# Optimization experiments

Measured on AMD Instinct MI355X. Metric: run time of the kernel, lower is better.

Reference implementation:

```python
import jax, jax.numpy as jnp
import numpy as np

N = 4096
C = 64
B = 4
DIST_THRESHOLD = 0.5
ALPHA = 0.01
NEG_INF = -1e15


def setup_inputs() -> dict:
    key = jax.random.key(0)
    k1, k2, k3, k4, k5 = jax.random.split(key, 5)
    x = jax.random.normal(k1, (B, N, C), dtype=jnp.float32)
    dist_mat = jax.random.uniform(k2, (N, N), dtype=jnp.float32)
    proj_w = jax.random.normal(k3, (N, C, C), dtype=jnp.float32) / np.sqrt(C)
    proj_b = jax.random.normal(k4, (N, C), dtype=jnp.float32) * 0.01
    a_w = jax.random.normal(k5, (N, 2 * C), dtype=jnp.float32) / np.sqrt(2 * C)
    return {"x": x, "dist_mat": dist_mat, "proj_w": proj_w, "proj_b": proj_b, "a_w": a_w}


def reference(x, dist_mat, proj_w, proj_b, a_w):
    # Adjacency: (0 < dist < threshold), diagonal forced to 1.
    adj = (dist_mat > 0) & (dist_mat < DIST_THRESHOLD)
    adj = adj | jnp.eye(N, dtype=bool)

    # Per-node projection (GraphDense): h[b,n,:] = x[b,n,:] @ proj_w[n] + proj_b[n]
    h = jnp.einsum('bnc,nco->bno', x, proj_w) + proj_b  # [B, N, C]

    # Attention score: a[j] . concat(h_i, h_j) without materializing [B,N,N,2C].
    a_src, a_dst = a_w[:, :C], a_w[:, C:]               # each [N, C]
    s = jnp.einsum('bic,jc->bij', h, a_src) + jnp.einsum('bjc,jc->bj', h, a_dst)[:, None, :]
    s = jnp.where(s >= 0, s, ALPHA * s)                 # LeakyReLU
    s = jnp.where(adj[None, :, :], s, NEG_INF)          # mask non-edges
    att = jax.nn.softmax(s, axis=-1)                    # [B, N, N]

    # Weighted aggregation over neighbors.
    y = jnp.einsum('bij,bjc->bic', att, h)              # [B, N, C]
    return y
```

## Files before the change

### kernel.cpp

```cpp
#include <hip/hip_runtime.h>

#define N 4096
#define C 64
#define B 4
#define SHIFT 12.0f

typedef __attribute__((ext_vector_type(8))) short short8;
typedef __attribute__((ext_vector_type(4))) short s16x4;
typedef __attribute__((ext_vector_type(4))) float f32x4;
typedef unsigned long long u64;

#define MFMA16(a, b, c) __builtin_amdgcn_mfma_f32_16x16x32_bf16(a, b, c, 0, 0, 0)

__device__ __forceinline__ short f2bf(float f) {
    unsigned u = __builtin_bit_cast(unsigned, f);
    u += 0x7fffu + ((u >> 16) & 1u);
    return (short)(u >> 16);
}

__global__ __launch_bounds__(256) void mask_kernel(const float* __restrict__ dist,
                                                   u64* __restrict__ msk) {
    const int wave = threadIdx.x >> 6, lane = threadIdx.x & 63;
    const int i = blockIdx.x * 4 + wave;
    const float* row = dist + (size_t)i * N;
#pragma unroll 8
    for (int jb = 0; jb < N / 64; jb++) {
        float d = row[jb * 64 + lane];
        u64 m = __ballot(d > 0.f && d < 0.5f);
        int dj = i - jb * 64;
        if (dj >= 0 && dj < 64) m |= (1ull << dj);
        if (lane == 0) msk[(size_t)i * (N / 64) + jb] = m;
    }
}

__global__ __launch_bounds__(256) void proj_kernel(
    const float* __restrict__ x,
    const float* __restrict__ proj_w,
    const float* __restrict__ proj_b,
    const float* __restrict__ a_w,
    short* __restrict__ h_bf,
    short* __restrict__ a_srcb,
    float* __restrict__ e2)
{
    __shared__ float lds_x[4][B][C];

    const int tid = threadIdx.x;
    const int wave = tid >> 6;
    const int lane = tid & 63;
    const int g = lane >> 4;
    const int o4 = lane & 15;
    const int n = blockIdx.x * 4 + wave;
    const float* Wn = proj_w + (size_t)n * C * C;

#pragma unroll
    for (int b = 0; b < B; b++)
        lds_x[wave][b][lane] = x[((size_t)b * N + n) * C + lane];

    float4 wbuf[16];
#pragma unroll
    for (int p = 0; p < 16; p++)
        wbuf[p] = *(const float4*)(Wn + (p * 4 + g) * C + o4 * 4);

    float acc[B][4];
#pragma unroll
    for (int b = 0; b < B; b++)
#pragma unroll
        for (int r = 0; r < 4; r++) acc[b][r] = 0.f;

#pragma unroll
    for (int p = 0; p < 16; p++) {
        float xs[B];
#pragma unroll
        for (int b = 0; b < B; b++) xs[b] = lds_x[wave][b][p * 4 + g];
#pragma unroll
        for (int b = 0; b < B; b++) {
            acc[b][0] = fmaf(xs[b], wbuf[p].x, acc[b][0]);
            acc[b][1] = fmaf(xs[b], wbuf[p].y, acc[b][1]);
            acc[b][2] = fmaf(xs[b], wbuf[p].z, acc[b][2]);
            acc[b][3] = fmaf(xs[b], wbuf[p].w, acc[b][3]);
        }
    }

#pragma unroll
    for (int b = 0; b < B; b++)
#pragma unroll
        for (int r = 0; r < 4; r++) {
            acc[b][r] += __shfl_xor(acc[b][r], 16, 64);
            acc[b][r] += __shfl_xor(acc[b][r], 32, 64);
        }

    float4 pb4 = *(const float4*)(proj_b + (size_t)n * C + o4 * 4);
#pragma unroll
    for (int b = 0; b < B; b++) {
        acc[b][0] += pb4.x; acc[b][1] += pb4.y;
        acc[b][2] += pb4.z; acc[b][3] += pb4.w;
    }

    float hg[4];
#pragma unroll
    for (int r = 0; r < 4; r++) {
        float v01 = (g & 1) ? acc[1][r] : acc[0][r];
        float v23 = (g & 1) ? acc[3][r] : acc[2][r];
        hg[r] = (g & 2) ? v23 : v01;
    }

    {
        s16x4 hv;
#pragma unroll
        for (int r = 0; r < 4; r++) hv[r] = f2bf(hg[r]);
        *(s16x4*)&h_bf[((size_t)g * N + n) * C + o4 * 4] = hv;
    }

    if (g == 0) {
        float4 as4 = *(const float4*)(a_w + (size_t)n * 2 * C + o4 * 4);
        s16x4 av;
        av[0] = f2bf(as4.x); av[1] = f2bf(as4.y);
        av[2] = f2bf(as4.z); av[3] = f2bf(as4.w);
        *(s16x4*)&a_srcb[(size_t)n * C + o4 * 4] = av;
    }

    {
        float4 ad4 = *(const float4*)(a_w + (size_t)n * 2 * C + C + o4 * 4);
        float s = hg[0] * ad4.x + hg[1] * ad4.y + hg[2] * ad4.z + hg[3] * ad4.w;
        s += __shfl_xor(s, 1, 64);
        s += __shfl_xor(s, 2, 64);
        s += __shfl_xor(s, 4, 64);
        s += __shfl_xor(s, 8, 64);
        if (o4 == 0) e2[g * N + n] = s - SHIFT;
    }
}

__global__ __launch_bounds__(256) void transpose_kernel(const short* __restrict__ h_bf,
                                                        short* __restrict__ hT_bf) {
    __shared__ short tile[64][72];
    const int t = threadIdx.x;
    const int b = blockIdx.y;
    const int n0 = blockIdx.x * 64;
    {
        int r = t >> 2, cs = (t & 3) * 16;
        const short* src = h_bf + ((size_t)b * N + n0 + r) * C + cs;
#pragma unroll
        for (int q = 0; q < 4; q++)
            *(s16x4*)&tile[r][cs + q * 4] = *(const s16x4*)(src + q * 4);
    }
    __syncthreads();
    {
        int c = t >> 2, ns = (t & 3) * 16;
        short v[16];
#pragma unroll
        for (int k = 0; k < 16; k++) v[k] = tile[ns + k][c];
        short* dst = hT_bf + (size_t)b * C * N + (size_t)c * N + n0 + ns;
        *(short8*)dst = *(short8*)&v[0];
        *(short8*)(dst + 8) = *(short8*)&v[8];
    }
}

__global__ __launch_bounds__(256) void attn_kernel(
    const u64* __restrict__ msk,
    const short* __restrict__ h_bf,
    const short* __restrict__ hT_bf,
    const short* __restrict__ a_srcb,
    const float* __restrict__ e2,
    float* __restrict__ part_y,
    float* __restrict__ part_l,
    int JS, int S, int mode)
{
    __shared__ short lds_a[2][64][72];

    const int tid = threadIdx.x;
    const int wave = tid >> 6;
    const int lane = tid & 63;
    const int cl = lane & 15;
    const int rg = lane >> 4;
    const int rg8 = rg * 8;
    const int b = wave;
    const int sy = blockIdx.x % S;
    const int ix = blockIdx.x / S;
    const int i0 = ix * 32;
    const int jbeg = sy * JS;

    short8 bfr[2][2];
#pragma unroll
    for (int u = 0; u < 2; u++) {
        const short* hrow = h_bf + ((size_t)b * N + i0 + u * 16 + cl) * C;
        bfr[u][0] = *(const short8*)(hrow + rg8);
        bfr[u][1] = *(const short8*)(hrow + 32 + rg8);
    }

    const u64* mr0 = msk + (size_t)(i0 + cl) * (N / 64);
    const u64* mr1 = msk + (size_t)(i0 + 16 + cl) * (N / 64);

    f32x4 yacc[2][4];
#pragma unroll
    for (int u = 0; u < 2; u++)
#pragma unroll
        for (int t = 0; t < 4; t++) { f32x4 z = {0.f, 0.f, 0.f, 0.f}; yacc[u][t] = z; }
    f32x4 yl[2];
    { f32x4 z = {0.f, 0.f, 0.f, 0.f}; yl[0] = z; yl[1] = z; }

    short8 ones;
#pragma unroll
    for (int k = 0; k < 8; k++) ones[k] = (short)0x3F80;

    const float* eb = e2 + (size_t)b * N;
    const short* hp[4];
#pragma unroll
    for (int t = 0; t < 4; t++)
        hp[t] = hT_bf + (size_t)b * C * N + (size_t)(t * 16 + cl) * N + jbeg + rg8;

    const int jr = ((cl >> 2) << 3) | (cl & 3);
    const int srow = tid >> 2, scol = (tid & 3) * 16;

    {
        short8 g0 = *(const short8*)(a_srcb + (size_t)jbeg * 64 + tid * 16);
        short8 g1 = *(const short8*)(a_srcb + (size_t)jbeg * 64 + tid * 16 + 8);
        *(short8*)&lds_a[0][srow][scol] = g0;
        *(short8*)&lds_a[0][srow][scol + 8] = g1;
    }
    __syncthreads();
    int buf = 0;

    for (int j0 = jbeg; j0 < jbeg + JS; j0 += 64) {
        const bool more = (j0 + 64 < jbeg + JS);
        const int jp = more ? j0 + 64 : j0;
        short8 g0 = *(const short8*)(a_srcb + (size_t)jp * 64 + tid * 16);
        short8 g1 = *(const short8*)(a_srcb + (size_t)jp * 64 + tid * 16 + 8);

        const u64 mbs0 = mr0[j0 >> 6], mbs1 = mr1[j0 >> 6];

        short8 pa[2][2];
#pragma unroll
        for (int u = 0; u < 2; u++) {
            const u64 mb = u ? mbs1 : mbs0;
            f32x4 st[4];
#pragma unroll
            for (int t = 0; t < 4; t++) {
                const int tq = t >> 1, tr = t & 1;
                const int vrow = jr + tq * 32 + tr * 4;
                short8 a0 = *(const short8*)&lds_a[buf][vrow][rg8];
                short8 a1 = *(const short8*)&lds_a[buf][vrow][32 + rg8];
                f32x4 eq = *(const f32x4*)(eb + j0 + tq * 32 + tr * 4 + rg8);
                unsigned w32 = tq ? (unsigned)(mb >> 32) : (unsigned)mb;
                unsigned ws = w32 >> (rg8 + tr * 4);
                f32x4 z;
#pragma unroll
                for (int r = 0; r < 4; r++)
                    z[r] = ((ws >> r) & 1u) ? eq[r] : -1e30f;
                z = MFMA16(a0, bfr[u][0], z);
                z = MFMA16(a1, bfr[u][1], z);
                st[t] = z;
            }

            short8 q0, q1;
#pragma unroll
            for (int t = 0; t < 4; t++) {
#pragma unroll
                for (int r = 0; r < 4; r++) {
                    float sv = st[t][r];
                    float pv = __expf(fmaxf(sv, fmaf(0.01f, sv, -11.88f)));
                    short bv = f2bf(pv);
                    if (t < 2) q0[(t & 1) * 4 + r] = bv;
                    else       q1[(t & 1) * 4 + r] = bv;
                }
            }
            pa[u][0] = q0;
            pa[u][1] = q1;

            yl[u] = MFMA16(pa[u][0], ones, yl[u]);
            yl[u] = MFMA16(pa[u][1], ones, yl[u]);
        }

        if (more) {
            *(short8*)&lds_a[buf ^ 1][srow][scol] = g0;
            *(short8*)&lds_a[buf ^ 1][srow][scol + 8] = g1;
        }
        __syncthreads();

#pragma unroll
        for (int t = 0; t < 4; t++) {
            short8 h0 = *(const short8*)(hp[t]);
            short8 h1 = *(const short8*)(hp[t] + 32);
            yacc[0][t] = MFMA16(pa[0][0], h0, yacc[0][t]);
            yacc[0][t] = MFMA16(pa[0][1], h1, yacc[0][t]);
            yacc[1][t] = MFMA16(pa[1][0], h0, yacc[1][t]);
            yacc[1][t] = MFMA16(pa[1][1], h1, yacc[1][t]);
            hp[t] += 64;
        }
        buf ^= 1;
    }

    if (mode) {
#pragma unroll
        for (int u = 0; u < 2; u++) {
            f32x4 inv;
#pragma unroll
            for (int r = 0; r < 4; r++) inv[r] = 1.f / yl[u][r];
#pragma unroll
            for (int t = 0; t < 4; t++)
#pragma unroll
                for (int r = 0; r < 4; r++)
                    part_y[((size_t)b * N + i0 + u * 16 + rg * 4 + r) * C + t * 16 + cl] =
                        yacc[u][t][r] * inv[r];
        }
    } else {
        size_t sb = (size_t)(sy * B + b) * N;
#pragma unroll
        for (int u = 0; u < 2; u++) {
#pragma unroll
            for (int t = 0; t < 4; t++)
#pragma unroll
                for (int r = 0; r < 4; r++)
                    part_y[(sb + i0 + u * 16 + rg * 4 + r) * C + t * 16 + cl] = yacc[u][t][r];
            if (cl == 0) *(f32x4*)&part_l[sb + i0 + u * 16 + rg * 4] = yl[u];
        }
    }
}

__global__ __launch_bounds__(256) void combine_kernel(
    const float* __restrict__ part_y, const float* __restrict__ part_l,
    float* __restrict__ out, int S)
{
    int g = blockIdx.x * 256 + threadIdx.x;
    int c4 = (g & 15) * 4;
    int row = (g >> 4) & (N - 1);
    int b = g >> 16;
    int bn = b * N + row;
    f32x4 y = {0.f, 0.f, 0.f, 0.f};
    float l = 0.f;
    if (S == 8) {
#pragma unroll
        for (int s = 0; s < 8; s++) {
            l += part_l[s * (B * N) + bn];
            f32x4 v = *(const f32x4*)&part_y[((size_t)s * B * N + bn) * C + c4];
#pragma unroll
            for (int r = 0; r < 4; r++) y[r] += v[r];
        }
    } else {
        for (int s = 0; s < S; s++) {
            l += part_l[s * (B * N) + bn];
            f32x4 v = *(const f32x4*)&part_y[((size_t)s * B * N + bn) * C + c4];
#pragma unroll
            for (int r = 0; r < 4; r++) y[r] += v[r];
        }
    }
    float inv = 1.f / l;
    f32x4 o;
#pragma unroll
    for (int r = 0; r < 4; r++) o[r] = y[r] * inv;
    *(f32x4*)&out[(size_t)g * 4] = o;
}

extern "C" void kernel_launch(void* const* d_in, const int* in_sizes, int n_in,
                              void* d_out, int out_size, void* d_ws, size_t ws_size,
                              hipStream_t stream) {
    const float* x      = (const float*)d_in[0];
    const float* dist   = (const float*)d_in[1];
    const float* proj_w = (const float*)d_in[2];
    const float* proj_b = (const float*)d_in[3];
    const float* a_w    = (const float*)d_in[4];
    float* out = (float*)d_out;

    char* ws = (char*)d_ws;
    short* h_bf   = (short*)(ws);
    short* hT_bf  = (short*)(ws + (2u << 20));
    short* a_srcb = (short*)(ws + (4u << 20));
    float* e2     = (float*)(ws + (4u << 20) + (512u << 10));
    u64*   msk    = (u64*)  (ws + (5u << 20));
    float* part_l = (float*)(ws + (7u << 20));
    float* part_y = (float*)(ws + (8u << 20));

    proj_kernel<<<N / 4, 256, 0, stream>>>(x, proj_w, proj_b, a_w, h_bf, a_srcb, e2);
    transpose_kernel<<<dim3(N / 64, B), 256, 0, stream>>>(h_bf, hT_bf);
    mask_kernel<<<N / 4, 256, 0, stream>>>(dist, msk);

    int S = 8;
    while (S > 1 && (8u << 20) + (size_t)S * B * N * C * 4 > ws_size) S >>= 1;
    bool direct = ((8u << 20) + (size_t)B * N * C * 4 > ws_size);

    if (direct) {
        attn_kernel<<<N / 32, 256, 0, stream>>>(
            msk, h_bf, hT_bf, a_srcb, e2, out, part_l, N, 1, 1);
    } else {
        attn_kernel<<<(N / 32) * S, 256, 0, stream>>>(
            msk, h_bf, hT_bf, a_srcb, e2, part_y, part_l, N / S, S, 0);
        combine_kernel<<<(B * N * C / 4) / 256, 256, 0, stream>>>(part_y, part_l, out, S);
    }
}
```

Measured before the change: 266.1 us.

## Stage a_src in 256-row LDS chunks instead of double-buffered 64-row tiles

```diff
diff --git a/kernel.cpp b/kernel.cpp
--- a/kernel.cpp
+++ b/kernel.cpp
@@ -4,6 +4,7 @@
 #define C 64
 #define B 4
 #define SHIFT 12.0f
+#define CH 256
 
 typedef __attribute__((ext_vector_type(8))) short short8;
 typedef __attribute__((ext_vector_type(4))) short s16x4;
@@ -165,7 +166,7 @@
     float* __restrict__ part_l,
     int JS, int S, int mode)
 {
-    __shared__ short lds_a[2][64][72];
+    __shared__ short lds_a[CH][72];
 
     const int tid = threadIdx.x;
     const int wave = tid >> 6;
@@ -209,84 +210,75 @@
         hp[t] = hT_bf + (size_t)b * C * N + (size_t)(t * 16 + cl) * N + jbeg + rg8;
 
     const int jr = ((cl >> 2) << 3) | (cl & 3);
-    const int srow = tid >> 2, scol = (tid & 3) * 16;
-
-    {
-        short8 g0 = *(const short8*)(a_srcb + (size_t)jbeg * 64 + tid * 16);
-        short8 g1 = *(const short8*)(a_srcb + (size_t)jbeg * 64 + tid * 16 + 8);
-        *(short8*)&lds_a[0][srow][scol] = g0;
-        *(short8*)&lds_a[0][srow][scol + 8] = g1;
-    }
-    __syncthreads();
-    int buf = 0;
-
-    for (int j0 = jbeg; j0 < jbeg + JS; j0 += 64) {
-        const bool more = (j0 + 64 < jbeg + JS);
-        const int jp = more ? j0 + 64 : j0;
-        short8 g0 = *(const short8*)(a_srcb + (size_t)jp * 64 + tid * 16);
-        short8 g1 = *(const short8*)(a_srcb + (size_t)jp * 64 + tid * 16 + 8);
-
-        const u64 mbs0 = mr0[j0 >> 6], mbs1 = mr1[j0 >> 6];
-
-        short8 pa[2][2];
-#pragma unroll
-        for (int u = 0; u < 2; u++) {
-            const u64 mb = u ? mbs1 : mbs0;
-            f32x4 st[4];
+
+    for (int c0 = jbeg; c0 < jbeg + JS; c0 += CH) {
+        __syncthreads();
+#pragma unroll 8
+        for (int q = 0; q < 8; q++) {
+            int idx = q * 256 + tid;
+            int row = idx >> 3, col = (idx & 7) * 8;
+            *(short8*)&lds_a[row][col] =
+                *(const short8*)(a_srcb + (size_t)c0 * 64 + idx * 8);
+        }
+        __syncthreads();
+
+        for (int j0 = c0; j0 < c0 + CH; j0 += 64) {
+            const int jl = j0 - c0;
+            const u64 mbs0 = mr0[j0 >> 6], mbs1 = mr1[j0 >> 6];
+
+            short8 pa[2][2];
+#pragma unroll
+            for (int u = 0; u < 2; u++) {
+                const u64 mb = u ? mbs1 : mbs0;
+                f32x4 st[4];
+#pragma unroll
+                for (int t = 0; t < 4; t++) {
+                    const int tq = t >> 1, tr = t & 1;
+                    const int vrow = jl + jr + tq * 32 + tr * 4;
+                    short8 a0 = *(const short8*)&lds_a[vrow][rg8];
+                    short8 a1 = *(const short8*)&lds_a[vrow][32 + rg8];
+                    f32x4 eq = *(const f32x4*)(eb + j0 + tq * 32 + tr * 4 + rg8);
+                    unsigned w32 = tq ? (unsigned)(mb >> 32) : (unsigned)mb;
+                    unsigned ws = w32 >> (rg8 + tr * 4);
+                    f32x4 z;
+#pragma unroll
+                    for (int r = 0; r < 4; r++)
+                        z[r] = ((ws >> r) & 1u) ? eq[r] : -1e30f;
+                    z = MFMA16(a0, bfr[u][0], z);
+                    z = MFMA16(a1, bfr[u][1], z);
+                    st[t] = z;
+                }
+
+                short8 q0, q1;
+#pragma unroll
+                for (int t = 0; t < 4; t++) {
+#pragma unroll
+                    for (int r = 0; r < 4; r++) {
+                        float sv = st[t][r];
+                        float pv = __expf(fmaxf(sv, fmaf(0.01f, sv, -11.88f)));
+                        short bv = f2bf(pv);
+                        if (t < 2) q0[(t & 1) * 4 + r] = bv;
+                        else       q1[(t & 1) * 4 + r] = bv;
+                    }
+                }
+                pa[u][0] = q0;
+                pa[u][1] = q1;
+
+                yl[u] = MFMA16(pa[u][0], ones, yl[u]);
+                yl[u] = MFMA16(pa[u][1], ones, yl[u]);
+            }
+
 #pragma unroll
             for (int t = 0; t < 4; t++) {
-                const int tq = t >> 1, tr = t & 1;
-                const int vrow = jr + tq * 32 + tr * 4;
-                short8 a0 = *(const short8*)&lds_a[buf][vrow][rg8];
-                short8 a1 = *(const short8*)&lds_a[buf][vrow][32 + rg8];
-                f32x4 eq = *(const f32x4*)(eb + j0 + tq * 32 + tr * 4 + rg8);
-                unsigned w32 = tq ? (unsigned)(mb >> 32) : (unsigned)mb;
-                unsigned ws = w32 >> (rg8 + tr * 4);
-                f32x4 z;
-#pragma unroll
-                for (int r = 0; r < 4; r++)
-                    z[r] = ((ws >> r) & 1u) ? eq[r] : -1e30f;
-                z = MFMA16(a0, bfr[u][0], z);
-                z = MFMA16(a1, bfr[u][1], z);
-                st[t] = z;
+                short8 h0 = *(const short8*)(hp[t]);
+                short8 h1 = *(const short8*)(hp[t] + 32);
+                yacc[0][t] = MFMA16(pa[0][0], h0, yacc[0][t]);
+                yacc[0][t] = MFMA16(pa[0][1], h1, yacc[0][t]);
+                yacc[1][t] = MFMA16(pa[1][0], h0, yacc[1][t]);
+                yacc[1][t] = MFMA16(pa[1][1], h1, yacc[1][t]);
+                hp[t] += 64;
             }
-
-            short8 q0, q1;
-#pragma unroll
-            for (int t = 0; t < 4; t++) {
-#pragma unroll
-                for (int r = 0; r < 4; r++) {
-                    float sv = st[t][r];
-                    float pv = __expf(fmaxf(sv, fmaf(0.01f, sv, -11.88f)));
-                    short bv = f2bf(pv);
-                    if (t < 2) q0[(t & 1) * 4 + r] = bv;
-                    else       q1[(t & 1) * 4 + r] = bv;
-                }
-            }
-            pa[u][0] = q0;
-            pa[u][1] = q1;
-
-            yl[u] = MFMA16(pa[u][0], ones, yl[u]);
-            yl[u] = MFMA16(pa[u][1], ones, yl[u]);
-        }
-
-        if (more) {
-            *(short8*)&lds_a[buf ^ 1][srow][scol] = g0;
-            *(short8*)&lds_a[buf ^ 1][srow][scol + 8] = g1;
-        }
-        __syncthreads();
-
-#pragma unroll
-        for (int t = 0; t < 4; t++) {
-            short8 h0 = *(const short8*)(hp[t]);
-            short8 h1 = *(const short8*)(hp[t] + 32);
-            yacc[0][t] = MFMA16(pa[0][0], h0, yacc[0][t]);
-            yacc[0][t] = MFMA16(pa[0][1], h1, yacc[0][t]);
-            yacc[1][t] = MFMA16(pa[1][0], h0, yacc[1][t]);
-            yacc[1][t] = MFMA16(pa[1][1], h1, yacc[1][t]);
-            hp[t] += 64;
-        }
-        buf ^= 1;
+        }
     }
 
     if (mode) {
```

Measured after the change: 258.2 us. 3.0% less time.
